# Kernel optimization log

Hardware: AMD Instinct MI355X
Metric: run time of the kernel (lower is better)

The kernel has to match this reference:

```python
import jax, jax.numpy as jnp
import numpy as np

B, T, C = 2, 2048, 1024
N_HEAD = 16
HEAD_DIM = C // N_HEAD


def setup_inputs() -> dict:
    key = jax.random.key(0)
    ks = jax.random.split(key, 5)
    s = 0.02
    return {
        "x": jax.random.normal(ks[0], (B, T, C), dtype=jnp.float32),
        "Wq": jax.random.normal(ks[1], (C, C), dtype=jnp.float32) * s,
        "bq": jnp.zeros((C,), dtype=jnp.float32),
        "Wk": jax.random.normal(ks[2], (C, C), dtype=jnp.float32) * s,
        "bk": jnp.zeros((C,), dtype=jnp.float32),
        "Wv": jax.random.normal(ks[3], (C, C), dtype=jnp.float32) * s,
        "bv": jnp.zeros((C,), dtype=jnp.float32),
        "Wo": jax.random.normal(ks[4], (C, C), dtype=jnp.float32) * s,
        "bo": jnp.zeros((C,), dtype=jnp.float32),
    }


def reference(x, Wq, bq, Wk, bk, Wv, bv, Wo, bo):
    b, t, c = x.shape
    h, d = N_HEAD, HEAD_DIM
    # projections -> [B, H, T, D]
    def proj(W, bias):
        return (x @ W.T + bias).reshape(b, t, h, d).transpose(0, 2, 1, 3)
    q = proj(Wq, bq)
    k = proj(Wk, bk)
    v = proj(Wv, bv)
    att = jnp.einsum("bhqd,bhkd->bhqk", q, k) / jnp.sqrt(jnp.float32(d))
    causal = jnp.tril(jnp.ones((t, t), dtype=bool))
    att = jnp.where(causal, att, jnp.float32(-jnp.inf))
    att = jax.nn.softmax(att, axis=-1)
    y = jnp.einsum("bhqk,bhkd->bhqd", att, v)  # [B,H,T,D]
    y = y.transpose(0, 2, 1, 3).reshape(b, t, c)
    return y @ Wo.T + bo
```

## Files before the change

### kernel.cpp

```cpp
#include <hip/hip_runtime.h>
#include <hip/hip_bf16.h>


namespace {

constexpr int TT = 2048;
constexpr int CC = 1024;
constexpr int HH = 16;
constexpr int DD = 64;

using bf16x8 = __attribute__((ext_vector_type(8))) __bf16;
using bf16x4 = __attribute__((ext_vector_type(4))) __bf16;
using f32x4  = __attribute__((ext_vector_type(4))) float;
using us8    = __attribute__((ext_vector_type(8))) unsigned short;

__device__ __forceinline__ unsigned short f2b(float f) {
  unsigned u = __float_as_uint(f);
  u += 0x7fffu + ((u >> 16) & 1u);
  return (unsigned short)(u >> 16);
}

__device__ __forceinline__ void gload16(const void* g, void* l) {
  __builtin_amdgcn_global_load_lds(
      (const __attribute__((address_space(1))) void*)g,
      (__attribute__((address_space(3))) void*)l, 16, 0, 0);
}

#if __has_builtin(__builtin_amdgcn_exp2f)
#define FEXP2 __builtin_amdgcn_exp2f
#else
#define FEXP2 exp2f
#endif

#define SCALE2 0.18033688011112042f

}

__global__ void k_cvt_all(const float* __restrict__ x,
                          const float* __restrict__ wq, const float* __restrict__ wk,
                          const float* __restrict__ wv, const float* __restrict__ wo,
                          unsigned short* __restrict__ dst) {
  const int i = blockIdx.x * 256 + threadIdx.x;
  const float* src; int off;
  if (i < 1048576)      { src = x;  off = i; }
  else if (i < 1310720) { src = wq; off = i - 1048576; }
  else if (i < 1572864) { src = wk; off = i - 1310720; }
  else if (i < 1835008) { src = wv; off = i - 1572864; }
  else                  { src = wo; off = i - 1835008; }
  float4 v = reinterpret_cast<const float4*>(src)[off];
  ushort4 o;
  o.x = f2b(v.x); o.y = f2b(v.y); o.z = f2b(v.z); o.w = f2b(v.w);
  reinterpret_cast<ushort4*>(dst)[i] = o;
}

__global__ __launch_bounds__(256, 3) void k_gemm_qkv(
    const unsigned short* __restrict__ A,
    const unsigned short* __restrict__ Wq,
    const unsigned short* __restrict__ Wk,
    const unsigned short* __restrict__ Wv,
    const float* __restrict__ bq,
    const float* __restrict__ bk,
    const float* __restrict__ bv,
    unsigned short* __restrict__ qd,
    unsigned short* __restrict__ kd,
    unsigned short* __restrict__ vd)
{
  __shared__ unsigned short la[2][128 * 32];
  __shared__ unsigned short lb[2][128 * 32];
  const int tid = threadIdx.x;
  const int lane = tid & 63;
  const int wid = tid >> 6;
  const int l15 = lane & 15, lg = lane >> 4;
  const int wm = (wid & 1) * 64, wn = (wid >> 1) * 64;
  const int bm = blockIdx.x;
  const int wsel = blockIdx.y >> 3;
  const int bnl = blockIdx.y & 7;

  const unsigned short* W = (wsel == 0) ? Wq : (wsel == 1) ? Wk : Wv;
  const float* bias = (wsel == 0) ? bq : (wsel == 1) ? bk : bv;

  const int srow = lane >> 2;
  const int sko  = (lane & 3) * 8;

  auto STAGE = [&](int buf, int kt) {
#pragma unroll
    for (int s = 0; s < 2; ++s) {
      const int seg = wid * 2 + s;
      const int row = seg * 16 + srow;
      gload16(&A[(bm * 128 + row) * CC + kt * 32 + sko], &la[buf][seg * 512]);
      gload16(&W[(bnl * 128 + row) * CC + kt * 32 + sko], &lb[buf][seg * 512]);
    }
  };

  f32x4 acc[4][4];
#pragma unroll
  for (int i = 0; i < 4; ++i)
#pragma unroll
    for (int j = 0; j < 4; ++j) acc[i][j] = f32x4{0.f, 0.f, 0.f, 0.f};

  auto COMPUTE = [&](int buf) {
    bf16x8 af[4], bf[4];
#pragma unroll
    for (int mi = 0; mi < 4; ++mi)
      af[mi] = __builtin_bit_cast(bf16x8,
        *reinterpret_cast<const us8*>(&la[buf][(wm + mi * 16 + l15) * 32 + lg * 8]));
#pragma unroll
    for (int ni = 0; ni < 4; ++ni)
      bf[ni] = __builtin_bit_cast(bf16x8,
        *reinterpret_cast<const us8*>(&lb[buf][(wn + ni * 16 + l15) * 32 + lg * 8]));
#pragma unroll
    for (int mi = 0; mi < 4; ++mi)
#pragma unroll
      for (int ni = 0; ni < 4; ++ni)
        acc[mi][ni] = __builtin_amdgcn_mfma_f32_16x16x32_bf16(af[mi], bf[ni], acc[mi][ni], 0, 0, 0);
  };

  STAGE(0, 0);
  STAGE(1, 1);
  int cur = 0;
  for (int kt = 0; kt < CC / 32 - 1; ++kt) {
    asm volatile("s_waitcnt vmcnt(4)" ::: "memory");
    __builtin_amdgcn_s_barrier();
    COMPUTE(cur);
    __builtin_amdgcn_s_barrier();
    if (kt < CC / 32 - 2) STAGE(cur, kt + 2);
    cur ^= 1;
  }
  asm volatile("s_waitcnt vmcnt(0)" ::: "memory");
  __builtin_amdgcn_s_barrier();
  COMPUTE(cur);

#pragma unroll
  for (int ni = 0; ni < 4; ++ni) {
    const int nl = bnl * 128 + wn + ni * 16 + l15;
    const float bvl = bias[nl];
    const int hh = nl >> 6, d = nl & (DD - 1);
#pragma unroll
    for (int mi = 0; mi < 4; ++mi) {
#pragma unroll
      for (int r = 0; r < 4; ++r) {
        const int m = bm * 128 + wm + mi * 16 + lg * 4 + r;
        float val = acc[mi][ni][r] + bvl;
        if (wsel == 0) val *= SCALE2;
        const unsigned short bb = f2b(val);
        const int b = m >> 11, t = m & (TT - 1);
        if (wsel == 0)
          qd[((b * HH + hh) * TT + t) * DD + d] = bb;
        else if (wsel == 1)
          kd[((b * HH + hh) * TT + t) * DD + d] = bb;
        else
          vd[((b * HH + hh) * DD + d) * TT + t] = bb;
      }
    }
  }
}

__global__ __launch_bounds__(256, 2) void k_gemm_o(
    const unsigned short* __restrict__ A,
    const unsigned short* __restrict__ W,
    const float* __restrict__ bias,
    float* __restrict__ out)
{
  __shared__ unsigned short la[2][128 * 32];
  __shared__ unsigned short lb[2][64 * 32];
  const int tid = threadIdx.x;
  const int lane = tid & 63;
  const int wid = tid >> 6;
  const int l15 = lane & 15, lg = lane >> 4;
  const int wm = (wid & 1) * 64, wn = (wid >> 1) * 32;
  const int bm = blockIdx.x, bn = blockIdx.y;

  const int srow = lane >> 2;
  const int sko  = (lane & 3) * 8;

  auto STAGE = [&](int buf, int kt) {
#pragma unroll
    for (int s = 0; s < 2; ++s) {
      const int seg = wid * 2 + s;
      gload16(&A[(bm * 128 + seg * 16 + srow) * CC + kt * 32 + sko], &la[buf][seg * 512]);
    }
    gload16(&W[(bn * 64 + wid * 16 + srow) * CC + kt * 32 + sko], &lb[buf][wid * 512]);
  };

  f32x4 acc[4][2];
#pragma unroll
  for (int i = 0; i < 4; ++i)
#pragma unroll
    for (int j = 0; j < 2; ++j) acc[i][j] = f32x4{0.f, 0.f, 0.f, 0.f};

  auto COMPUTE = [&](int buf) {
    bf16x8 af[4], bf[2];
#pragma unroll
    for (int mi = 0; mi < 4; ++mi)
      af[mi] = __builtin_bit_cast(bf16x8,
        *reinterpret_cast<const us8*>(&la[buf][(wm + mi * 16 + l15) * 32 + lg * 8]));
#pragma unroll
    for (int ni = 0; ni < 2; ++ni)
      bf[ni] = __builtin_bit_cast(bf16x8,
        *reinterpret_cast<const us8*>(&lb[buf][(wn + ni * 16 + l15) * 32 + lg * 8]));
#pragma unroll
    for (int mi = 0; mi < 4; ++mi)
#pragma unroll
      for (int ni = 0; ni < 2; ++ni)
        acc[mi][ni] = __builtin_amdgcn_mfma_f32_16x16x32_bf16(af[mi], bf[ni], acc[mi][ni], 0, 0, 0);
  };

  STAGE(0, 0);
  STAGE(1, 1);
  int cur = 0;
  for (int kt = 0; kt < CC / 32 - 1; ++kt) {
    asm volatile("s_waitcnt vmcnt(3)" ::: "memory");
    __builtin_amdgcn_s_barrier();
    COMPUTE(cur);
    __builtin_amdgcn_s_barrier();
    if (kt < CC / 32 - 2) STAGE(cur, kt + 2);
    cur ^= 1;
  }
  asm volatile("s_waitcnt vmcnt(0)" ::: "memory");
  __builtin_amdgcn_s_barrier();
  COMPUTE(cur);

#pragma unroll
  for (int ni = 0; ni < 2; ++ni) {
    const int n = bn * 64 + wn + ni * 16 + l15;
    const float bvl = bias[n];
#pragma unroll
    for (int mi = 0; mi < 4; ++mi)
#pragma unroll
      for (int r = 0; r < 4; ++r) {
        const int m = bm * 128 + wm + mi * 16 + lg * 4 + r;
        out[m * CC + n] = acc[mi][ni][r] + bvl;
      }
  }
}

__global__ __launch_bounds__(64) void k_attn(
    const unsigned short* __restrict__ Q,
    const unsigned short* __restrict__ K,
    const unsigned short* __restrict__ VT,
    unsigned short* __restrict__ Y)
{
  __shared__ unsigned short pl[2][2][16][80];
  const int lane = threadIdx.x;
  const int l15 = lane & 15, lg = lane >> 4;
  const int wg = blockIdx.x + 32 * blockIdx.y;
  const int swz = (wg & 7) * 128 + (wg >> 3);
  const int p = swz & 31;
  const int bh = swz >> 5;
  const int b = bh >> 4, h = bh & 15;
  const int qb0A = p * 32;
  const int qb0B = (63 - p) * 32;
  const int nktA = (qb0A + 95) >> 6;
  const int nktB = (qb0B + 95) >> 6;

  const unsigned short* Qh = Q + bh * TT * DD;
  const unsigned short* Kh = K + bh * TT * DD;
  const unsigned short* Vh = VT + bh * DD * TT;

  auto ldq = [&](bf16x8 (&qf)[2][2], int qb0) {
#pragma unroll
    for (int qi = 0; qi < 2; ++qi)
#pragma unroll
      for (int kk = 0; kk < 2; ++kk)
        qf[qi][kk] = __builtin_bit_cast(bf16x8,
          *reinterpret_cast<const us8*>(&Qh[(qb0 + qi * 16 + l15) * DD + kk * 32 + lg * 8]));
  };

  bf16x8 qfA[2][2], qfB[2][2];
  ldq(qfA, qb0A); ldq(qfB, qb0B);

  f32x4 oA[2][4], oB[2][4];
  float mrA[2], lrA[2], mrB[2], lrB[2];
#pragma unroll
  for (int qi = 0; qi < 2; ++qi) {
    mrA[qi] = -INFINITY; lrA[qi] = 0.f;
    mrB[qi] = -INFINITY; lrB[qi] = 0.f;
#pragma unroll
    for (int dc = 0; dc < 4; ++dc) {
      oA[qi][dc] = f32x4{0.f, 0.f, 0.f, 0.f};
      oB[qi][dc] = f32x4{0.f, 0.f, 0.f, 0.f};
    }
  }

  for (int kt = 0; kt < nktB; ++kt) {
    const int kbase = kt * 64;
    bf16x8 kf[4][2], vf[2][4];
#pragma unroll
    for (int f = 0; f < 4; ++f)
#pragma unroll
      for (int kk = 0; kk < 2; ++kk)
        kf[f][kk] = __builtin_bit_cast(bf16x8,
          *reinterpret_cast<const us8*>(&Kh[(kbase + f * 16 + l15) * DD + kk * 32 + lg * 8]));
#pragma unroll
    for (int kk = 0; kk < 2; ++kk)
#pragma unroll
      for (int dc = 0; dc < 4; ++dc)
        vf[kk][dc] = __builtin_bit_cast(bf16x8,
          *reinterpret_cast<const us8*>(&Vh[(dc * 16 + l15) * TT + kbase + kk * 32 + lg * 8]));

    const bool doA = (kt < nktA);

    auto qk_sm = [&](const bf16x8 (&qf)[2][2], const int qb0, float (&mr)[2],
                     float (&lr)[2], f32x4 (&o)[2][4],
                     unsigned short (&plS)[2][16][80]) {
      f32x4 s[2][4];
#pragma unroll
      for (int qi = 0; qi < 2; ++qi)
#pragma unroll
        for (int f = 0; f < 4; ++f) {
          f32x4 t0 = __builtin_amdgcn_mfma_f32_16x16x32_bf16(kf[f][0], qf[qi][0],
                                                             f32x4{0.f,0.f,0.f,0.f}, 0, 0, 0);
          s[qi][f] = __builtin_amdgcn_mfma_f32_16x16x32_bf16(kf[f][1], qf[qi][1], t0, 0, 0, 0);
        }
      const bool needMask = (kbase + 63 > qb0);
#pragma unroll
      for (int qi = 0; qi < 2; ++qi) {
        const int qg = qb0 + qi * 16 + l15;
        float mt = -INFINITY;
#pragma unroll
        for (int f = 0; f < 4; ++f)
#pragma unroll
          for (int r = 0; r < 4; ++r) {
            float v = s[qi][f][r];
            if (needMask) v = (kbase + f * 16 + lg * 4 + r <= qg) ? v : -INFINITY;
            s[qi][f][r] = v;
            mt = fmaxf(mt, v);
          }
        mt = fmaxf(mt, __shfl_xor(mt, 16));
        mt = fmaxf(mt, __shfl_xor(mt, 32));
        const float mn = fmaxf(mr[qi], mt);
        const float al = FEXP2(mr[qi] - mn);
        mr[qi] = mn;
        float rs = 0.f;
#pragma unroll
        for (int f = 0; f < 4; ++f) {
          const float p0 = FEXP2(s[qi][f][0] - mn), p1 = FEXP2(s[qi][f][1] - mn);
          const float p2 = FEXP2(s[qi][f][2] - mn), p3 = FEXP2(s[qi][f][3] - mn);
          rs += (p0 + p1) + (p2 + p3);
          bf16x4 pk;
          pk[0] = (__bf16)p0; pk[1] = (__bf16)p1; pk[2] = (__bf16)p2; pk[3] = (__bf16)p3;
          *reinterpret_cast<bf16x4*>(&plS[qi][l15][f * 16 + lg * 4]) = pk;
        }
        rs += __shfl_xor(rs, 16);
        rs += __shfl_xor(rs, 32);
        lr[qi] = lr[qi] * al + rs;
#pragma unroll
        for (int dc = 0; dc < 4; ++dc)
#pragma unroll
          for (int r = 0; r < 4; ++r) o[qi][dc][r] *= al;
      }
    };

    qk_sm(qfB, qb0B, mrB, lrB, oB, pl[0]);
    if (doA) qk_sm(qfA, qb0A, mrA, lrA, oA, pl[1]);

    asm volatile("s_waitcnt lgkmcnt(0)" ::: "memory");
    __builtin_amdgcn_sched_barrier(0);

    auto pv = [&](f32x4 (&o)[2][4], unsigned short (&plS)[2][16][80]) {
#pragma unroll
      for (int qi = 0; qi < 2; ++qi) {
        const bf16x8 pa0 = __builtin_bit_cast(bf16x8,
          *reinterpret_cast<const us8*>(&plS[qi][l15][lg * 8]));
        const bf16x8 pa1 = __builtin_bit_cast(bf16x8,
          *reinterpret_cast<const us8*>(&plS[qi][l15][32 + lg * 8]));
#pragma unroll
        for (int dc = 0; dc < 4; ++dc) {
          o[qi][dc] = __builtin_amdgcn_mfma_f32_16x16x32_bf16(vf[0][dc], pa0, o[qi][dc], 0, 0, 0);
          o[qi][dc] = __builtin_amdgcn_mfma_f32_16x16x32_bf16(vf[1][dc], pa1, o[qi][dc], 0, 0, 0);
        }
      }
    };
    pv(oB, pl[0]);
    if (doA) pv(oA, pl[1]);
  }

  auto epi = [&](int qb0, f32x4 (&o)[2][4], float (&lr)[2]) {
#pragma unroll
    for (int qi = 0; qi < 2; ++qi) {
      const float linv = 1.f / lr[qi];
      const int t = qb0 + qi * 16 + l15;
#pragma unroll
      for (int dc = 0; dc < 4; ++dc) {
        bf16x4 pk;
#pragma unroll
        for (int r = 0; r < 4; ++r)
          pk[r] = __builtin_bit_cast(__bf16, f2b(o[qi][dc][r] * linv));
        *reinterpret_cast<bf16x4*>(
            &Y[(b * TT + t) * CC + h * DD + dc * 16 + lg * 4]) = pk;
      }
    }
  };
  epi(qb0B, oB, lrB);
  epi(qb0A, oA, lrA);
}

extern "C" void kernel_launch(void* const* d_in, const int* in_sizes, int n_in,
                              void* d_out, int out_size, void* d_ws, size_t ws_size,
                              hipStream_t stream) {
  const float* x  = (const float*)d_in[0];
  const float* Wq = (const float*)d_in[1];
  const float* bq = (const float*)d_in[2];
  const float* Wk = (const float*)d_in[3];
  const float* bk = (const float*)d_in[4];
  const float* Wv = (const float*)d_in[5];
  const float* bv = (const float*)d_in[6];
  const float* Wo = (const float*)d_in[7];
  const float* bo = (const float*)d_in[8];
  float* out = (float*)d_out;

  unsigned short* ws  = (unsigned short*)d_ws;
  unsigned short* xb  = ws;
  unsigned short* wqb = xb  + 4194304;
  unsigned short* wkb = wqb + 1048576;
  unsigned short* wvb = wkb + 1048576;
  unsigned short* wob = wvb + 1048576;
  unsigned short* qb  = wob + 1048576;
  unsigned short* kb  = qb  + 4194304;
  unsigned short* vt  = kb  + 4194304;
  unsigned short* yb  = xb;

  k_cvt_all<<<8192, 256, 0, stream>>>(x, Wq, Wk, Wv, Wo, ws);

  k_gemm_qkv<<<dim3(32, 24), 256, 0, stream>>>(xb, wqb, wkb, wvb, bq, bk, bv, qb, kb, vt);

  k_attn<<<dim3(32, 32), 64, 0, stream>>>(qb, kb, vt, yb);

  k_gemm_o<<<dim3(32, 16), 256, 0, stream>>>(yb, wob, bo, out);
}
```

Baseline: 210.3 us.

## Switch attention kernel to 32x32x16 MFMA tiles with K prefetch double-buffering

Rewrites the attention inner loop to use 32x32x16 bf16 MFMA instructions instead of 16x16x32, so each wave processes a 32-row query block per tile with one softmax row per lane-half. The cross-lane reductions shrink to a single shuffle and the P tile layout in LDS changes to match. K fragments for the next tile are loaded into a second register buffer while the current tile is computed, which manually unrolls the loop by two. This raises register pressure and adds loads clamped to the last tile.

Result: no change. 206.8 us (-1.7%).

```diff
diff --git a/kernel.cpp b/kernel.cpp
--- a/kernel.cpp
+++ b/kernel.cpp
@@ -12,6 +12,7 @@
 using bf16x8 = __attribute__((ext_vector_type(8))) __bf16;
 using bf16x4 = __attribute__((ext_vector_type(4))) __bf16;
 using f32x4  = __attribute__((ext_vector_type(4))) float;
+using f32x16 = __attribute__((ext_vector_type(16))) float;
 using us8    = __attribute__((ext_vector_type(8))) unsigned short;
 
 __device__ __forceinline__ unsigned short f2b(float f) {
@@ -240,9 +241,11 @@
     const unsigned short* __restrict__ VT,
     unsigned short* __restrict__ Y)
 {
-  __shared__ unsigned short pl[2][2][16][80];
+  __shared__ unsigned short pl[2][32][68];
   const int lane = threadIdx.x;
-  const int l15 = lane & 15, lg = lane >> 4;
+  const int l31 = lane & 31;
+  const int hi = lane >> 5;
+  const int klane = hi * 4;
   const int wg = blockIdx.x + 32 * blockIdx.y;
   const int swz = (wg & 7) * 128 + (wg >> 3);
   const int p = swz & 31;
@@ -257,142 +260,150 @@
   const unsigned short* Kh = K + bh * TT * DD;
   const unsigned short* Vh = VT + bh * DD * TT;
 
-  auto ldq = [&](bf16x8 (&qf)[2][2], int qb0) {
-#pragma unroll
-    for (int qi = 0; qi < 2; ++qi)
-#pragma unroll
-      for (int kk = 0; kk < 2; ++kk)
-        qf[qi][kk] = __builtin_bit_cast(bf16x8,
-          *reinterpret_cast<const us8*>(&Qh[(qb0 + qi * 16 + l15) * DD + kk * 32 + lg * 8]));
-  };
-
-  bf16x8 qfA[2][2], qfB[2][2];
-  ldq(qfA, qb0A); ldq(qfB, qb0B);
-
-  f32x4 oA[2][4], oB[2][4];
-  float mrA[2], lrA[2], mrB[2], lrB[2];
-#pragma unroll
-  for (int qi = 0; qi < 2; ++qi) {
-    mrA[qi] = -INFINITY; lrA[qi] = 0.f;
-    mrB[qi] = -INFINITY; lrB[qi] = 0.f;
-#pragma unroll
-    for (int dc = 0; dc < 4; ++dc) {
-      oA[qi][dc] = f32x4{0.f, 0.f, 0.f, 0.f};
-      oB[qi][dc] = f32x4{0.f, 0.f, 0.f, 0.f};
-    }
-  }
-
-  for (int kt = 0; kt < nktB; ++kt) {
-    const int kbase = kt * 64;
-    bf16x8 kf[4][2], vf[2][4];
-#pragma unroll
-    for (int f = 0; f < 4; ++f)
-#pragma unroll
-      for (int kk = 0; kk < 2; ++kk)
-        kf[f][kk] = __builtin_bit_cast(bf16x8,
-          *reinterpret_cast<const us8*>(&Kh[(kbase + f * 16 + l15) * DD + kk * 32 + lg * 8]));
-#pragma unroll
-    for (int kk = 0; kk < 2; ++kk)
-#pragma unroll
-      for (int dc = 0; dc < 4; ++dc)
-        vf[kk][dc] = __builtin_bit_cast(bf16x8,
-          *reinterpret_cast<const us8*>(&Vh[(dc * 16 + l15) * TT + kbase + kk * 32 + lg * 8]));
-
-    const bool doA = (kt < nktA);
-
-    auto qk_sm = [&](const bf16x8 (&qf)[2][2], const int qb0, float (&mr)[2],
-                     float (&lr)[2], f32x4 (&o)[2][4],
-                     unsigned short (&plS)[2][16][80]) {
-      f32x4 s[2][4];
-#pragma unroll
-      for (int qi = 0; qi < 2; ++qi)
-#pragma unroll
-        for (int f = 0; f < 4; ++f) {
-          f32x4 t0 = __builtin_amdgcn_mfma_f32_16x16x32_bf16(kf[f][0], qf[qi][0],
-                                                             f32x4{0.f,0.f,0.f,0.f}, 0, 0, 0);
-          s[qi][f] = __builtin_amdgcn_mfma_f32_16x16x32_bf16(kf[f][1], qf[qi][1], t0, 0, 0, 0);
-        }
-      const bool needMask = (kbase + 63 > qb0);
-#pragma unroll
-      for (int qi = 0; qi < 2; ++qi) {
-        const int qg = qb0 + qi * 16 + l15;
-        float mt = -INFINITY;
-#pragma unroll
-        for (int f = 0; f < 4; ++f)
-#pragma unroll
-          for (int r = 0; r < 4; ++r) {
-            float v = s[qi][f][r];
-            if (needMask) v = (kbase + f * 16 + lg * 4 + r <= qg) ? v : -INFINITY;
-            s[qi][f][r] = v;
-            mt = fmaxf(mt, v);
-          }
-        mt = fmaxf(mt, __shfl_xor(mt, 16));
-        mt = fmaxf(mt, __shfl_xor(mt, 32));
-        const float mn = fmaxf(mr[qi], mt);
-        const float al = FEXP2(mr[qi] - mn);
-        mr[qi] = mn;
-        float rs = 0.f;
-#pragma unroll
-        for (int f = 0; f < 4; ++f) {
-          const float p0 = FEXP2(s[qi][f][0] - mn), p1 = FEXP2(s[qi][f][1] - mn);
-          const float p2 = FEXP2(s[qi][f][2] - mn), p3 = FEXP2(s[qi][f][3] - mn);
-          rs += (p0 + p1) + (p2 + p3);
-          bf16x4 pk;
-          pk[0] = (__bf16)p0; pk[1] = (__bf16)p1; pk[2] = (__bf16)p2; pk[3] = (__bf16)p3;
-          *reinterpret_cast<bf16x4*>(&plS[qi][l15][f * 16 + lg * 4]) = pk;
-        }
-        rs += __shfl_xor(rs, 16);
-        rs += __shfl_xor(rs, 32);
-        lr[qi] = lr[qi] * al + rs;
-#pragma unroll
-        for (int dc = 0; dc < 4; ++dc)
-#pragma unroll
-          for (int r = 0; r < 4; ++r) o[qi][dc][r] *= al;
+  bf16x8 qfA[4], qfB[4];
+#pragma unroll
+  for (int dk = 0; dk < 4; ++dk) {
+    qfA[dk] = __builtin_bit_cast(bf16x8,
+      *reinterpret_cast<const us8*>(&Qh[(qb0A + l31) * DD + dk * 16 + hi * 8]));
+    qfB[dk] = __builtin_bit_cast(bf16x8,
+      *reinterpret_cast<const us8*>(&Qh[(qb0B + l31) * DD + dk * 16 + hi * 8]));
+  }
+
+  f32x16 oA0, oA1, oB0, oB1;
+#pragma unroll
+  for (int r = 0; r < 16; ++r) { oA0[r] = 0.f; oA1[r] = 0.f; oB0[r] = 0.f; oB1[r] = 0.f; }
+  float mrA = -INFINITY, lrA = 0.f, mrB = -INFINITY, lrB = 0.f;
+
+  auto ldk = [&](bf16x8 (&kf)[2][4], int kb_base) {
+#pragma unroll
+    for (int kb = 0; kb < 2; ++kb)
+#pragma unroll
+      for (int dk = 0; dk < 4; ++dk)
+        kf[kb][dk] = __builtin_bit_cast(bf16x8,
+          *reinterpret_cast<const us8*>(&Kh[(kb_base + kb * 32 + l31) * DD + dk * 16 + hi * 8]));
+  };
+  auto ldv = [&](bf16x8 (&vf)[2][4], int kb_base) {
+#pragma unroll
+    for (int dc = 0; dc < 2; ++dc)
+#pragma unroll
+      for (int kc = 0; kc < 4; ++kc)
+        vf[dc][kc] = __builtin_bit_cast(bf16x8,
+          *reinterpret_cast<const us8*>(&Vh[(dc * 32 + l31) * TT + kb_base + kc * 16 + hi * 8]));
+  };
+
+  auto qk_sm = [&](const bf16x8 (&kf)[2][4], const bf16x8 (&qf)[4], const int qb0,
+                   float& mr, float& lr, f32x16& o0, f32x16& o1,
+                   unsigned short (&plS)[32][68], const int kbase) {
+    f32x16 s0, s1;
+#pragma unroll
+    for (int r = 0; r < 16; ++r) { s0[r] = 0.f; s1[r] = 0.f; }
+#pragma unroll
+    for (int dk = 0; dk < 4; ++dk) {
+      s0 = __builtin_amdgcn_mfma_f32_32x32x16_bf16(kf[0][dk], qf[dk], s0, 0, 0, 0);
+      s1 = __builtin_amdgcn_mfma_f32_32x32x16_bf16(kf[1][dk], qf[dk], s1, 0, 0, 0);
+    }
+    const int qg = qb0 + l31;
+    if (kbase + 63 > qb0) {
+#pragma unroll
+      for (int r = 0; r < 16; ++r) {
+        const int kc0 = kbase + (r & 3) + 8 * (r >> 2) + klane;
+        s0[r] = (kc0 <= qg)      ? s0[r] : -INFINITY;
+        s1[r] = (kc0 + 32 <= qg) ? s1[r] : -INFINITY;
       }
-    };
-
-    qk_sm(qfB, qb0B, mrB, lrB, oB, pl[0]);
-    if (doA) qk_sm(qfA, qb0A, mrA, lrA, oA, pl[1]);
-
-    asm volatile("s_waitcnt lgkmcnt(0)" ::: "memory");
-    __builtin_amdgcn_sched_barrier(0);
-
-    auto pv = [&](f32x4 (&o)[2][4], unsigned short (&plS)[2][16][80]) {
-#pragma unroll
-      for (int qi = 0; qi < 2; ++qi) {
-        const bf16x8 pa0 = __builtin_bit_cast(bf16x8,
-          *reinterpret_cast<const us8*>(&plS[qi][l15][lg * 8]));
-        const bf16x8 pa1 = __builtin_bit_cast(bf16x8,
-          *reinterpret_cast<const us8*>(&plS[qi][l15][32 + lg * 8]));
-#pragma unroll
-        for (int dc = 0; dc < 4; ++dc) {
-          o[qi][dc] = __builtin_amdgcn_mfma_f32_16x16x32_bf16(vf[0][dc], pa0, o[qi][dc], 0, 0, 0);
-          o[qi][dc] = __builtin_amdgcn_mfma_f32_16x16x32_bf16(vf[1][dc], pa1, o[qi][dc], 0, 0, 0);
-        }
+    }
+    float ma = s0[0], mb = s1[0];
+#pragma unroll
+    for (int r = 1; r < 16; ++r) { ma = fmaxf(ma, s0[r]); mb = fmaxf(mb, s1[r]); }
+    float mt = fmaxf(ma, mb);
+    mt = fmaxf(mt, __shfl_xor(mt, 32));
+    const float mn = fmaxf(mr, mt);
+    const float al = FEXP2(mr - mn);
+    mr = mn;
+    float rs0 = 0.f, rs1 = 0.f;
+#pragma unroll
+    for (int g = 0; g < 4; ++g) {
+      const float a0 = FEXP2(s0[g * 4 + 0] - mn), a1 = FEXP2(s0[g * 4 + 1] - mn);
+      const float a2 = FEXP2(s0[g * 4 + 2] - mn), a3 = FEXP2(s0[g * 4 + 3] - mn);
+      rs0 += (a0 + a1) + (a2 + a3);
+      bf16x4 pk0;
+      pk0[0] = (__bf16)a0; pk0[1] = (__bf16)a1; pk0[2] = (__bf16)a2; pk0[3] = (__bf16)a3;
+      *reinterpret_cast<bf16x4*>(&plS[l31][g * 8 + klane]) = pk0;
+      const float b0 = FEXP2(s1[g * 4 + 0] - mn), b1 = FEXP2(s1[g * 4 + 1] - mn);
+      const float b2 = FEXP2(s1[g * 4 + 2] - mn), b3 = FEXP2(s1[g * 4 + 3] - mn);
+      rs1 += (b0 + b1) + (b2 + b3);
+      bf16x4 pk1;
+      pk1[0] = (__bf16)b0; pk1[1] = (__bf16)b1; pk1[2] = (__bf16)b2; pk1[3] = (__bf16)b3;
+      *reinterpret_cast<bf16x4*>(&plS[l31][32 + g * 8 + klane]) = pk1;
+    }
+    float rs = rs0 + rs1;
+    rs += __shfl_xor(rs, 32);
+    lr = lr * al + rs;
+    o0 *= al;
+    o1 *= al;
+  };
+
+  auto pv = [&](const bf16x8 (&vf)[2][4], f32x16& o0, f32x16& o1,
+                unsigned short (&plS)[32][68]) {
+#pragma unroll
+    for (int kc = 0; kc < 4; ++kc) {
+      const bf16x8 pa = __builtin_bit_cast(bf16x8,
+        *reinterpret_cast<const us8*>(&plS[l31][kc * 16 + hi * 8]));
+      o0 = __builtin_amdgcn_mfma_f32_32x32x16_bf16(vf[0][kc], pa, o0, 0, 0, 0);
+      o1 = __builtin_amdgcn_mfma_f32_32x32x16_bf16(vf[1][kc], pa, o1, 0, 0, 0);
+    }
+  };
+
+  bf16x8 kf0[2][4], kf1[2][4];
+  ldk(kf0, 0);
+  for (int kt = 0; kt < nktB; kt += 2) {
+    {
+      const int kbase = kt * 64;
+      bf16x8 vf[2][4];
+      ldv(vf, kbase);
+      const int nx1 = (kt + 1 < nktB) ? kt + 1 : nktB - 1;
+      ldk(kf1, nx1 * 64);
+      qk_sm(kf0, qfB, qb0B, mrB, lrB, oB0, oB1, pl[0], kbase);
+      const bool doA = (kt < nktA);
+      if (doA) qk_sm(kf0, qfA, qb0A, mrA, lrA, oA0, oA1, pl[1], kbase);
+      asm volatile("s_waitcnt lgkmcnt(0)" ::: "memory");
+      __builtin_amdgcn_sched_barrier(0);
+      pv(vf, oB0, oB1, pl[0]);
+      if (doA) pv(vf, oA0, oA1, pl[1]);
+    }
+    if (kt + 1 < nktB) {
+      const int kbase = (kt + 1) * 64;
+      bf16x8 vf[2][4];
+      ldv(vf, kbase);
+      const int nx2 = (kt + 2 < nktB) ? kt + 2 : nktB - 1;
+      ldk(kf0, nx2 * 64);
+      qk_sm(kf1, qfB, qb0B, mrB, lrB, oB0, oB1, pl[0], kbase);
+      const bool doA = (kt + 1 < nktA);
+      if (doA) qk_sm(kf1, qfA, qb0A, mrA, lrA, oA0, oA1, pl[1], kbase);
+      asm volatile("s_waitcnt lgkmcnt(0)" ::: "memory");
+      __builtin_amdgcn_sched_barrier(0);
+      pv(vf, oB0, oB1, pl[0]);
+      if (doA) pv(vf, oA0, oA1, pl[1]);
+    }
+  }
+
+  auto epi = [&](int qb0, const f32x16& o0, const f32x16& o1, float lr) {
+    const float linv = 1.f / lr;
+    const int t = qb0 + l31;
+    unsigned short* yrow = &Y[(b * TT + t) * CC + h * DD];
+#pragma unroll
+    for (int g = 0; g < 4; ++g) {
+      bf16x4 w0, w1;
+#pragma unroll
+      for (int i = 0; i < 4; ++i) {
+        w0[i] = __builtin_bit_cast(__bf16, f2b(o0[g * 4 + i] * linv));
+        w1[i] = __builtin_bit_cast(__bf16, f2b(o1[g * 4 + i] * linv));
       }
-    };
-    pv(oB, pl[0]);
-    if (doA) pv(oA, pl[1]);
-  }
-
-  auto epi = [&](int qb0, f32x4 (&o)[2][4], float (&lr)[2]) {
-#pragma unroll
-    for (int qi = 0; qi < 2; ++qi) {
-      const float linv = 1.f / lr[qi];
-      const int t = qb0 + qi * 16 + l15;
-#pragma unroll
-      for (int dc = 0; dc < 4; ++dc) {
-        bf16x4 pk;
-#pragma unroll
-        for (int r = 0; r < 4; ++r)
-          pk[r] = __builtin_bit_cast(__bf16, f2b(o[qi][dc][r] * linv));
-        *reinterpret_cast<bf16x4*>(
-            &Y[(b * TT + t) * CC + h * DD + dc * 16 + lg * 4]) = pk;
-      }
-    }
-  };
-  epi(qb0B, oB, lrB);
-  epi(qb0A, oA, lrA);
+      *reinterpret_cast<bf16x4*>(&yrow[g * 8 + klane]) = w0;
+      *reinterpret_cast<bf16x4*>(&yrow[32 + g * 8 + klane]) = w1;
+    }
+  };
+  epi(qb0B, oB0, oB1, lrB);
+  epi(qb0A, oA0, oA1, lrA);
 }
 
 extern "C" void kernel_launch(void* const* d_in, const int* in_sizes, int n_in,
```
